# Optimization experiments

Measured on AMD Instinct MI355X. Metric: run time of the kernel, lower is better.

## Reference

```python
import jax, jax.numpy as jnp
import numpy as np

N_WIRES = 8
DIM = 1 << N_WIRES  # 256

# --- static precompute: CNOT-ring basis permutation and PauliZ sign matrix ---
# torchquantum convention: wire 0 is the most significant bit of the basis index.
_gates = [(w, w + 1) for w in range(N_WIRES - 1)] + [(N_WIRES - 1, 0)]
_perm = np.empty(DIM, dtype=np.int64)
for b in range(DIM):
    bits = [(b >> (N_WIRES - 1 - w)) & 1 for w in range(N_WIRES)]
    for c, t in _gates:
        if bits[c]:
            bits[t] ^= 1
    _perm[b] = sum(bit << (N_WIRES - 1 - w) for w, bit in enumerate(bits))
_Z = np.array([[1.0 - 2.0 * ((idx >> (N_WIRES - 1 - w)) & 1) for w in range(N_WIRES)]
               for idx in range(DIM)], dtype=np.float32)
# exp_Z[w] = sum_b probs_in[b] * Z[perm[b], w]  (CNOTs permute basis states)
_M = jnp.asarray(_Z[_perm])  # [256, 8]


def _quantum_head(angles):
    """angles: [..., 8] RX angles -> PauliZ expectations [..., 8].

    Circuit: RX(angle_w) on each wire from |0>, CNOT ring, MeasureAll(PauliZ).
    Post-RX state is a product state; CNOTs only permute basis states, so
    probabilities suffice (no complex amplitudes needed).
    """
    half = angles * 0.5
    c2 = jnp.cos(half) ** 2  # P(qubit=0)
    s2 = jnp.sin(half) ** 2  # P(qubit=1)
    # Build the 256-dim joint probability vector via sequential outer products.
    p = jnp.ones(angles.shape[:-1] + (1,), angles.dtype)
    for w in range(N_WIRES):
        pw = jnp.stack([c2[..., w], s2[..., w]], axis=-1)  # [..., 2]
        p = (p[..., :, None] * pw[..., None, :]).reshape(angles.shape[:-1] + (-1,))
    return p @ _M.astype(p.dtype)  # [..., 8]


def setup_inputs() -> dict:
    key = jax.random.key(0)
    ks = jax.random.split(key, 6)
    B, S, E = 8, 512, 768
    scale = 1.0 / np.sqrt(E)
    return {
        "x": jax.random.normal(ks[0], (B, S, E), jnp.float32),
        "W_proj": jax.random.normal(ks[1], (E, E), jnp.float32) * scale,
        "b_proj": jax.random.normal(ks[2], (E,), jnp.float32) * 0.02,
        "theta": jax.random.normal(ks[3], (N_WIRES,), jnp.float32),
        "W_comb": jax.random.normal(ks[4], (E, E), jnp.float32) * scale,
        "b_comb": jax.random.normal(ks[5], (E,), jnp.float32) * 0.02,
    }


def reference(x, W_proj, b_proj, theta, W_comb, b_comb):
    B, S, E = x.shape
    H = E // N_WIRES  # num_heads = 96
    proj = x @ W_proj.T + b_proj                 # [B, S, E] (torch Linear)
    angles = proj.reshape(B, S, H, N_WIRES) + theta  # encoder RX(x) then RX(theta): angles add
    expz = _quantum_head(angles)                 # [B, S, H, 8]
    out = expz.reshape(B, S, E)                  # heads re-concatenated
    # dropout is identity in eval mode
    return out @ W_comb.T + b_comb
```

## Files before the change

kernel.cpp:

```cpp
#include <hip/hip_runtime.h>

typedef _Float16 v8h __attribute__((ext_vector_type(8)));
typedef float    v4f __attribute__((ext_vector_type(4)));

__device__ __forceinline__ void gl_lds16(const void* g, void* l) {
  __builtin_amdgcn_global_load_lds(
      (__attribute__((address_space(1))) void*)(void*)g,
      (__attribute__((address_space(3))) void*)l, 16, 0, 0);
}
__device__ __forceinline__ v8h cvt8(const float4 a, const float4 b) {
  v8h o;
  o[0] = (_Float16)a.x; o[1] = (_Float16)a.y; o[2] = (_Float16)a.z; o[3] = (_Float16)a.w;
  o[4] = (_Float16)b.x; o[5] = (_Float16)b.y; o[6] = (_Float16)b.z; o[7] = (_Float16)b.w;
  return o;
}

__global__ void conv_w(const float4* __restrict__ wp, const float4* __restrict__ wc,
                       v8h* __restrict__ op, v8h* __restrict__ oc) {
  const int n = 73728;
  int i = blockIdx.x * blockDim.x + threadIdx.x;
  const float4* src = (i < n) ? wp : wc;
  v8h* dst = (i < n) ? op : oc;
  const int j = (i < n) ? i : i - n;
  dst[j] = cvt8(src[2 * j], src[2 * j + 1]);
}


__global__ __launch_bounds__(256) void gemm1_qh(
    const float* __restrict__ X,
    const _Float16* __restrict__ B,
    const float* __restrict__ bp,
    const float* __restrict__ theta,
    _Float16* __restrict__ EZ) {
  const int t = threadIdx.x;
  const int b = blockIdx.x;
  const int xcd = b & 7, slot = b >> 3;
  const int bm = xcd * 8 + slot / 12;
  const int bn = slot % 12;

  const int wave = t >> 6, lane = t & 63;
  const int quad = lane >> 4, l16 = lane & 15;
  const int wm = (wave >> 1) * 32, wn = (wave & 1) * 32;

  __shared__ __align__(16) unsigned char smem[32768];
  _Float16* As = (_Float16*)smem;
  _Float16* Bs = (_Float16*)(smem + 16384);
  float* Cs = (float*)smem;

  const float4 th0 = *(const float4*)theta;
  const float4 th1 = *(const float4*)(theta + 4);

  const int tr = t >> 4;
  const int tc = t & 15;
  const int cgl = tc ^ tr;

  const float*    Xg = X + (size_t)(bm * 64 + tr) * 768 + cgl * 8;
  const _Float16* Bg = B + (size_t)(bn * 64 + tr) * 768 + cgl * 8;

  v4f acc[2][2];
#pragma unroll
  for (int i = 0; i < 2; i++)
#pragma unroll
    for (int j = 0; j < 2; j++) acc[i][j] = (v4f){0.f, 0.f, 0.f, 0.f};

  float4 xr[4][2];
#pragma unroll
  for (int c = 0; c < 4; c++) {
    const float* p = Xg + (size_t)c * 16 * 768;
    xr[c][0] = *(const float4*)p;
    xr[c][1] = *(const float4*)(p + 4);
  }

  for (int kt = 0; kt < 768; kt += 128) {
#pragma unroll
    for (int c = 0; c < 4; c++)
      gl_lds16(Bg + (size_t)c * 16 * 768 + kt, &Bs[c * 2048 + t * 8]);
#pragma unroll
    for (int c = 0; c < 4; c++)
      *(v8h*)&As[c * 2048 + t * 8] = cvt8(xr[c][0], xr[c][1]);
    __syncthreads();
    if (kt + 128 < 768) {
#pragma unroll
      for (int c = 0; c < 4; c++) {
        const float* p = Xg + (size_t)c * 16 * 768 + kt + 128;
        xr[c][0] = *(const float4*)p;
        xr[c][1] = *(const float4*)(p + 4);
      }
    }
#pragma unroll
    for (int q = 0; q < 4; q++) {
      v8h af[2], bf[2];
#pragma unroll
      for (int i = 0; i < 2; i++)
        af[i] = *(const v8h*)&As[(wm + i * 16 + l16) * 128 + (((q * 4 + quad) ^ l16) * 8)];
#pragma unroll
      for (int j = 0; j < 2; j++)
        bf[j] = *(const v8h*)&Bs[(wn + j * 16 + l16) * 128 + (((q * 4 + quad) ^ l16) * 8)];
#pragma unroll
      for (int i = 0; i < 2; i++)
#pragma unroll
        for (int j = 0; j < 2; j++)
          acc[i][j] = __builtin_amdgcn_mfma_f32_16x16x32_f16(af[i], bf[j], acc[i][j], 0, 0, 0);
    }
    __syncthreads();
  }

  const int r0 = wm + quad * 4;
  const int c0 = wn + l16;
#pragma unroll
  for (int j = 0; j < 2; j++)
#pragma unroll
    for (int i = 0; i < 2; i++)
#pragma unroll
      for (int r = 0; r < 4; r++)
        Cs[(r0 + i * 16 + r) * 68 + c0 + j * 16] = acc[i][j][r];
  __syncthreads();

#pragma unroll
  for (int s = 0; s < 2; s++) {
    const int idx = t + s * 256;
    const int row = idx >> 3, h = idx & 7;
    const int gcol = bn * 64 + h * 8;
    const float* cr = &Cs[row * 68 + h * 8];
    const float4 q0 = *(const float4*)cr;
    const float4 q1 = *(const float4*)(cr + 4);
    const float4 b0 = *(const float4*)(bp + gcol);
    const float4 b1 = *(const float4*)(bp + gcol + 4);
    float c[8];
    c[0] = cosf(q0.x + b0.x + th0.x);
    c[1] = cosf(q0.y + b0.y + th0.y);
    c[2] = cosf(q0.z + b0.z + th0.z);
    c[3] = cosf(q0.w + b0.w + th0.w);
    c[4] = cosf(q1.x + b1.x + th1.x);
    c[5] = cosf(q1.y + b1.y + th1.y);
    c[6] = cosf(q1.z + b1.z + th1.z);
    c[7] = cosf(q1.w + b1.w + th1.w);
    float e[8];
    e[0] = c[1] * c[2] * c[3] * c[4] * c[5] * c[6] * c[7];
    float pr = c[0];
#pragma unroll
    for (int w = 1; w < 8; w++) { pr *= c[w]; e[w] = pr; }
    v8h ov;
#pragma unroll
    for (int w = 0; w < 8; w++) ov[w] = (_Float16)e[w];
    *(v8h*)(EZ + (size_t)(bm * 64 + row) * 768 + gcol) = ov;
  }
}

__global__ __launch_bounds__(256) void gemm2(
    const _Float16* __restrict__ A,
    const _Float16* __restrict__ B,
    float* __restrict__ C,
    const float* __restrict__ bias) {
  const int t = threadIdx.x;
  const int b = blockIdx.x;
  const int xcd = b & 7, slot = b >> 3;
  const int bm = xcd * 8 + slot / 12;
  const int bn = slot % 12;

  const int wave = t >> 6, lane = t & 63;
  const int quad = lane >> 4, l16 = lane & 15;
  const int wm = (wave >> 1) * 32, wn = (wave & 1) * 32;

  __shared__ __align__(16) _Float16 As[64 * 128];
  __shared__ __align__(16) _Float16 Bs[64 * 128];

  const int tr = t >> 4;
  const int tc = t & 15;
  const int cgl = tc ^ tr;

  const _Float16* Ag = A + (size_t)(bm * 64 + tr) * 768 + cgl * 8;
  const _Float16* Bg = B + (size_t)(bn * 64 + tr) * 768 + cgl * 8;

  v4f acc[2][2];
#pragma unroll
  for (int i = 0; i < 2; i++)
#pragma unroll
    for (int j = 0; j < 2; j++) acc[i][j] = (v4f){0.f, 0.f, 0.f, 0.f};

  for (int kt = 0; kt < 768; kt += 128) {
#pragma unroll
    for (int c = 0; c < 4; c++) {
      gl_lds16(Ag + (size_t)c * 16 * 768 + kt, &As[c * 2048 + t * 8]);
      gl_lds16(Bg + (size_t)c * 16 * 768 + kt, &Bs[c * 2048 + t * 8]);
    }
    __syncthreads();
#pragma unroll
    for (int q = 0; q < 4; q++) {
      v8h af[2], bf[2];
#pragma unroll
      for (int i = 0; i < 2; i++)
        af[i] = *(const v8h*)&As[(wm + i * 16 + l16) * 128 + (((q * 4 + quad) ^ l16) * 8)];
#pragma unroll
      for (int j = 0; j < 2; j++)
        bf[j] = *(const v8h*)&Bs[(wn + j * 16 + l16) * 128 + (((q * 4 + quad) ^ l16) * 8)];
#pragma unroll
      for (int ii = 0; ii < 2; ii++)
#pragma unroll
        for (int j = 0; j < 2; j++)
          acc[ii][j] = __builtin_amdgcn_mfma_f32_16x16x32_f16(af[ii], bf[j], acc[ii][j], 0, 0, 0);
    }
    __syncthreads();
  }

  const int row0 = bm * 64 + wm + quad * 4;
  const int col0 = bn * 64 + wn + l16;
#pragma unroll
  for (int j = 0; j < 2; j++) {
    const int col = col0 + j * 16;
    const float bv = bias[col];
#pragma unroll
    for (int i = 0; i < 2; i++) {
#pragma unroll
      for (int r = 0; r < 4; r++) {
        C[(size_t)(row0 + i * 16 + r) * 768 + col] = acc[i][j][r] + bv;
      }
    }
  }
}

extern "C" void kernel_launch(void* const* d_in, const int* in_sizes, int n_in,
                              void* d_out, int out_size, void* d_ws, size_t ws_size,
                              hipStream_t stream) {
  const float* x     = (const float*)d_in[0];
  const float* Wp    = (const float*)d_in[1];
  const float* bp    = (const float*)d_in[2];
  const float* theta = (const float*)d_in[3];
  const float* Wcf   = (const float*)d_in[4];
  const float* bc    = (const float*)d_in[5];
  float* out = (float*)d_out;

  const size_t EE = (size_t)768 * 768;

  _Float16* WPH = (_Float16*)d_ws;
  _Float16* WCH = WPH + EE;
  _Float16* EZ  = WCH + EE;

  conv_w<<<(int)(2 * EE / 8 / 256), 256, 0, stream>>>(
      (const float4*)Wp, (const float4*)Wcf, (v8h*)WPH, (v8h*)WCH);

  gemm1_qh<<<768, 256, 0, stream>>>(x, WPH, bp, theta, EZ);

  gemm2<<<768, 256, 0, stream>>>(EZ, WCH, out, bc);
}
```

Baseline: 99.48 us.

## Double-buffer LDS tiles with K=64 stages in both GEMM kernels

Both GEMM kernels now split the 128-wide K tile into two 64-wide LDS buffers. The next tile (global_load_lds for B, and for A in gemm2; register-staged fp16-converted X in gemm1) is loaded into the alternate buffer while MFMAs consume the current one. The row/column swizzle is redone for 64-element rows. The aim is to overlap global-memory latency with compute instead of stalling at the barrier after each load. The trade-off is twice as many loop iterations and barriers, at the same 32 KB LDS footprint.

After: 99.33 us. No clear change (-0.2%).

```diff
diff --git a/kernel.cpp b/kernel.cpp
--- a/kernel.cpp
+++ b/kernel.cpp
@@ -43,19 +43,17 @@
   const int wm = (wave >> 1) * 32, wn = (wave & 1) * 32;
 
   __shared__ __align__(16) unsigned char smem[32768];
-  _Float16* As = (_Float16*)smem;
-  _Float16* Bs = (_Float16*)(smem + 16384);
   float* Cs = (float*)smem;
 
   const float4 th0 = *(const float4*)theta;
   const float4 th1 = *(const float4*)(theta + 4);
 
-  const int tr = t >> 4;
-  const int tc = t & 15;
-  const int cgl = tc ^ tr;
-
-  const float*    Xg = X + (size_t)(bm * 64 + tr) * 768 + cgl * 8;
-  const _Float16* Bg = B + (size_t)(bn * 64 + tr) * 768 + cgl * 8;
+  const int r = t >> 3;
+  const int cg = t & 7;
+  const int lcg = cg ^ (r & 7);
+
+  const float*    Xg = X + (size_t)(bm * 64 + r) * 768 + lcg * 8;
+  const _Float16* Bg = B + (size_t)(bn * 64 + r) * 768 + lcg * 8;
 
   v4f acc[2][2];
 #pragma unroll
@@ -63,39 +61,60 @@
 #pragma unroll
     for (int j = 0; j < 2; j++) acc[i][j] = (v4f){0.f, 0.f, 0.f, 0.f};
 
-  float4 xr[4][2];
-#pragma unroll
-  for (int c = 0; c < 4; c++) {
-    const float* p = Xg + (size_t)c * 16 * 768;
-    xr[c][0] = *(const float4*)p;
-    xr[c][1] = *(const float4*)(p + 4);
-  }
-
-  for (int kt = 0; kt < 768; kt += 128) {
-#pragma unroll
-    for (int c = 0; c < 4; c++)
-      gl_lds16(Bg + (size_t)c * 16 * 768 + kt, &Bs[c * 2048 + t * 8]);
-#pragma unroll
-    for (int c = 0; c < 4; c++)
-      *(v8h*)&As[c * 2048 + t * 8] = cvt8(xr[c][0], xr[c][1]);
-    __syncthreads();
-    if (kt + 128 < 768) {
-#pragma unroll
-      for (int c = 0; c < 4; c++) {
-        const float* p = Xg + (size_t)c * 16 * 768 + kt + 128;
-        xr[c][0] = *(const float4*)p;
-        xr[c][1] = *(const float4*)(p + 4);
+  float4 xr[4];
+#pragma unroll
+  for (int c = 0; c < 2; c++) {
+    const float* p = Xg + (size_t)c * 32 * 768;
+    xr[2 * c]     = *(const float4*)p;
+    xr[2 * c + 1] = *(const float4*)(p + 4);
+  }
+  {
+    _Float16* B0 = (_Float16*)(smem + 16384);
+    gl_lds16(Bg, &B0[t * 8]);
+    gl_lds16(Bg + (size_t)32 * 768, &B0[2048 + t * 8]);
+    _Float16* A0 = (_Float16*)smem;
+    *(v8h*)&A0[t * 8]        = cvt8(xr[0], xr[1]);
+    *(v8h*)&A0[2048 + t * 8] = cvt8(xr[2], xr[3]);
+  }
+#pragma unroll
+  for (int c = 0; c < 2; c++) {
+    const float* p = Xg + (size_t)c * 32 * 768 + 64;
+    xr[2 * c]     = *(const float4*)p;
+    xr[2 * c + 1] = *(const float4*)(p + 4);
+  }
+  __syncthreads();
+
+#pragma unroll
+  for (int it = 0; it < 12; ++it) {
+    _Float16* Ac = (_Float16*)(smem + (it & 1) * 8192);
+    _Float16* Bc = (_Float16*)(smem + 16384 + (it & 1) * 8192);
+    if (it < 11) {
+      _Float16* An = (_Float16*)(smem + ((it + 1) & 1) * 8192);
+      _Float16* Bn = (_Float16*)(smem + 16384 + ((it + 1) & 1) * 8192);
+      const int kn = (it + 1) * 64;
+      gl_lds16(Bg + kn, &Bn[t * 8]);
+      gl_lds16(Bg + (size_t)32 * 768 + kn, &Bn[2048 + t * 8]);
+      *(v8h*)&An[t * 8]        = cvt8(xr[0], xr[1]);
+      *(v8h*)&An[2048 + t * 8] = cvt8(xr[2], xr[3]);
+      if (it < 10) {
+        const int kf = (it + 2) * 64;
+#pragma unroll
+        for (int c = 0; c < 2; c++) {
+          const float* p = Xg + (size_t)c * 32 * 768 + kf;
+          xr[2 * c]     = *(const float4*)p;
+          xr[2 * c + 1] = *(const float4*)(p + 4);
+        }
       }
     }
 #pragma unroll
-    for (int q = 0; q < 4; q++) {
+    for (int q = 0; q < 2; q++) {
       v8h af[2], bf[2];
 #pragma unroll
       for (int i = 0; i < 2; i++)
-        af[i] = *(const v8h*)&As[(wm + i * 16 + l16) * 128 + (((q * 4 + quad) ^ l16) * 8)];
+        af[i] = *(const v8h*)&Ac[(wm + i * 16 + l16) * 64 + ((((q << 2) + quad) ^ (l16 & 7)) << 3)];
 #pragma unroll
       for (int j = 0; j < 2; j++)
-        bf[j] = *(const v8h*)&Bs[(wn + j * 16 + l16) * 128 + (((q * 4 + quad) ^ l16) * 8)];
+        bf[j] = *(const v8h*)&Bc[(wn + j * 16 + l16) * 64 + ((((q << 2) + quad) ^ (l16 & 7)) << 3)];
 #pragma unroll
       for (int i = 0; i < 2; i++)
 #pragma unroll
@@ -112,8 +131,8 @@
 #pragma unroll
     for (int i = 0; i < 2; i++)
 #pragma unroll
-      for (int r = 0; r < 4; r++)
-        Cs[(r0 + i * 16 + r) * 68 + c0 + j * 16] = acc[i][j][r];
+      for (int rr = 0; rr < 4; rr++)
+        Cs[(r0 + i * 16 + rr) * 68 + c0 + j * 16] = acc[i][j][rr];
   __syncthreads();
 
 #pragma unroll
@@ -162,15 +181,14 @@
   const int quad = lane >> 4, l16 = lane & 15;
   const int wm = (wave >> 1) * 32, wn = (wave & 1) * 32;
 
-  __shared__ __align__(16) _Float16 As[64 * 128];
-  __shared__ __align__(16) _Float16 Bs[64 * 128];
-
-  const int tr = t >> 4;
-  const int tc = t & 15;
-  const int cgl = tc ^ tr;
-
-  const _Float16* Ag = A + (size_t)(bm * 64 + tr) * 768 + cgl * 8;
-  const _Float16* Bg = B + (size_t)(bn * 64 + tr) * 768 + cgl * 8;
+  __shared__ __align__(16) unsigned char smem[32768];
+
+  const int r = t >> 3;
+  const int cg = t & 7;
+  const int lcg = cg ^ (r & 7);
+
+  const _Float16* Ag = A + (size_t)(bm * 64 + r) * 768 + lcg * 8;
+  const _Float16* Bg = B + (size_t)(bn * 64 + r) * 768 + lcg * 8;
 
   v4f acc[2][2];
 #pragma unroll
@@ -178,22 +196,38 @@
 #pragma unroll
     for (int j = 0; j < 2; j++) acc[i][j] = (v4f){0.f, 0.f, 0.f, 0.f};
 
-  for (int kt = 0; kt < 768; kt += 128) {
-#pragma unroll
-    for (int c = 0; c < 4; c++) {
-      gl_lds16(Ag + (size_t)c * 16 * 768 + kt, &As[c * 2048 + t * 8]);
-      gl_lds16(Bg + (size_t)c * 16 * 768 + kt, &Bs[c * 2048 + t * 8]);
-    }
-    __syncthreads();
-#pragma unroll
-    for (int q = 0; q < 4; q++) {
+  {
+    _Float16* A0 = (_Float16*)smem;
+    _Float16* B0 = (_Float16*)(smem + 16384);
+    gl_lds16(Ag, &A0[t * 8]);
+    gl_lds16(Ag + (size_t)32 * 768, &A0[2048 + t * 8]);
+    gl_lds16(Bg, &B0[t * 8]);
+    gl_lds16(Bg + (size_t)32 * 768, &B0[2048 + t * 8]);
+  }
+  __syncthreads();
+
+#pragma unroll
+  for (int it = 0; it < 12; ++it) {
+    _Float16* Ac = (_Float16*)(smem + (it & 1) * 8192);
+    _Float16* Bc = (_Float16*)(smem + 16384 + (it & 1) * 8192);
+    if (it < 11) {
+      _Float16* An = (_Float16*)(smem + ((it + 1) & 1) * 8192);
+      _Float16* Bn = (_Float16*)(smem + 16384 + ((it + 1) & 1) * 8192);
+      const int kn = (it + 1) * 64;
+      gl_lds16(Ag + kn, &An[t * 8]);
+      gl_lds16(Ag + (size_t)32 * 768 + kn, &An[2048 + t * 8]);
+      gl_lds16(Bg + kn, &Bn[t * 8]);
+      gl_lds16(Bg + (size_t)32 * 768 + kn, &Bn[2048 + t * 8]);
+    }
+#pragma unroll
+    for (int q = 0; q < 2; q++) {
       v8h af[2], bf[2];
 #pragma unroll
       for (int i = 0; i < 2; i++)
-        af[i] = *(const v8h*)&As[(wm + i * 16 + l16) * 128 + (((q * 4 + quad) ^ l16) * 8)];
+        af[i] = *(const v8h*)&Ac[(wm + i * 16 + l16) * 64 + ((((q << 2) + quad) ^ (l16 & 7)) << 3)];
 #pragma unroll
       for (int j = 0; j < 2; j++)
-        bf[j] = *(const v8h*)&Bs[(wn + j * 16 + l16) * 128 + (((q * 4 + quad) ^ l16) * 8)];
+        bf[j] = *(const v8h*)&Bc[(wn + j * 16 + l16) * 64 + ((((q << 2) + quad) ^ (l16 & 7)) << 3)];
 #pragma unroll
       for (int ii = 0; ii < 2; ii++)
 #pragma unroll
@@ -212,8 +246,8 @@
 #pragma unroll
     for (int i = 0; i < 2; i++) {
 #pragma unroll
-      for (int r = 0; r < 4; r++) {
-        C[(size_t)(row0 + i * 16 + r) * 768 + col] = acc[i][j][r] + bv;
+      for (int rr = 0; rr < 4; rr++) {
+        C[(size_t)(row0 + i * 16 + rr) * 768 + col] = acc[i][j][rr] + bv;
       }
     }
   }
```
